# Optimization experiments

Hardware: AMD Instinct MI355X
Metric: run time of the kernel (lower is better)

The kernel has to match this reference:

```python
import jax, jax.numpy as jnp
import numpy as np

DIM = 2048
N_HEADS = 16
HEAD_DIM = DIM // N_HEADS
EPS = 1e-6


def setup_inputs() -> dict:
    key = jax.random.key(0)
    k1, k2, k3, k4, k5 = jax.random.split(key, 5)
    B, S = 2, 2048
    x = jax.random.normal(k1, (B, S, DIM), dtype=jnp.float32)
    cos = jax.random.uniform(k2, (S, HEAD_DIM), dtype=jnp.float32)
    sin = jax.random.uniform(k3, (S, HEAD_DIM), dtype=jnp.float32)
    # torch nn.Linear convention: weight [out_features, in_features], y = x @ W.T
    W_qkv = jax.random.normal(k4, (3 * DIM, DIM), dtype=jnp.float32) * 0.02
    W_proj = jax.random.normal(k5, (DIM, DIM), dtype=jnp.float32) * 0.02
    return {"x": x, "cos": cos, "sin": sin, "W_qkv": W_qkv, "W_proj": W_proj}


def _apply_rope(x, cos, sin):
    # x: [B,H,S,D], cos/sin: [S,D]; rotate interleaved even/odd pairs
    x1, x2 = x[..., ::2], x[..., 1::2]
    c = cos[:, ::2][None, None]  # [1,1,S,D/2]
    s = sin[:, ::2][None, None]
    y1 = x1 * c - x2 * s
    y2 = x1 * s + x2 * c
    return jnp.stack([y1, y2], axis=-1).reshape(x.shape)


def _rms_norm(x):
    # per-head RMS normalization over last dim, no learned scale
    return x * jax.lax.rsqrt(jnp.mean(x * x, axis=-1, keepdims=True) + EPS)


def reference(x, cos, sin, W_qkv, W_proj):
    b, s, d = x.shape
    qkv = jnp.einsum('bsd,ed->bse', x, W_qkv)  # [B,S,3*dim]
    q, k, v = jnp.split(qkv, 3, axis=-1)
    # [B,S,dim] -> [B,H,S,Dh]
    def to_heads(t):
        return t.reshape(b, s, N_HEADS, HEAD_DIM).transpose(0, 2, 1, 3)
    q, k, v = to_heads(q), to_heads(k), to_heads(v)
    q = _apply_rope(_rms_norm(q), cos, sin)
    k = _apply_rope(_rms_norm(k), cos, sin)
    scale = 1.0 / jnp.sqrt(jnp.asarray(HEAD_DIM, dtype=x.dtype))
    scores = jnp.einsum('bhqd,bhkd->bhqk', q, k) * scale  # [B,H,S,S]
    attn = jax.nn.softmax(scores, axis=-1)
    out = jnp.einsum('bhqk,bhkd->bhqd', attn, v)  # [B,H,S,Dh]
    out = out.transpose(0, 2, 1, 3).reshape(b, s, d)
    return jnp.einsum('bsd,od->bso', out, W_proj)
```

## Files before the change

kernel.cpp:

```cpp
#include <hip/hip_runtime.h>
#include <math.h>

#define BATCH 2
#define SEQ   2048
#define DIM   2048
#define NH    16
#define HD    128
#define EPS   1e-6f

typedef _Float16 f16x8 __attribute__((ext_vector_type(8)));
typedef _Float16 f16x4 __attribute__((ext_vector_type(4)));
typedef _Float16 f16x2 __attribute__((ext_vector_type(2)));
typedef float    f32x4 __attribute__((ext_vector_type(4)));

#define MFMA_F16 __builtin_amdgcn_mfma_f32_16x16x32_f16

__global__ __launch_bounds__(256) void cvt_f16(
    const float* __restrict__ in, _Float16* __restrict__ out) {
  int i = blockIdx.x * 256 + threadIdx.x;
  float4 v = ((const float4*)in)[i];
  f16x4 o;
  o[0] = (_Float16)v.x; o[1] = (_Float16)v.y;
  o[2] = (_Float16)v.z; o[3] = (_Float16)v.w;
  ((f16x4*)out)[i] = o;
}

__global__ __launch_bounds__(512, 2) void gemm_1p(
    const _Float16* __restrict__ Ag, const _Float16* __restrict__ Bg,
    float* __restrict__ C, int M, int N, int K) {
  __shared__ __align__(16) _Float16 smem[2][384][64];

  const int t = threadIdx.x;
  const int w = t >> 6, lane = t & 63;
  const int bm = blockIdx.y * 128, bn = blockIdx.x * 256;
  const int wr = (w >> 2) * 64;
  const int wc = (w & 3) * 64;
  const int quad = lane >> 4, c15 = lane & 15;

  const _Float16* baseA = Ag + (size_t)bm * K;
  const _Float16* baseB = Bg + (size_t)bn * K;

  const int lrow = lane >> 3;
  const int lswz = ((lane & 7) ^ lrow) * 8;

  const int col0 = ((0 + quad) ^ (c15 & 7)) * 8;
  const int col1 = ((4 + quad) ^ (c15 & 7)) * 8;

  f32x4 acc[4][4] = {};
  f16x8 a0[4], b0[4], a1[4], b1[4];

#define STAGE_TILE(buf, kofs)                                                  \
  {                                                                            \
    _Pragma("unroll")                                                          \
    for (int e = 0; e < 6; ++e) {                                              \
      int c = w * 6 + e;                                                       \
      int rl = c * 8 + lrow;                                                   \
      const _Float16* g = (rl < 128) ? (baseA + (size_t)rl * K)                \
                                     : (baseB + (size_t)(rl - 128) * K);       \
      __builtin_amdgcn_global_load_lds(                                        \
          (const __attribute__((address_space(1))) unsigned int*)(g + (kofs) + lswz), \
          (__attribute__((address_space(3))) unsigned int*)(&smem[buf][c * 8][0]),    \
          16, 0, 0);                                                           \
    }                                                                          \
  }

#define RD(dstA, dstB, colv, buf)                                              \
  _Pragma("unroll")                                                            \
  for (int m2 = 0; m2 < 4; ++m2)                                               \
    dstA[m2] = *(const f16x8*)(&smem[buf][wr + m2 * 16 + c15][colv]);          \
  _Pragma("unroll")                                                            \
  for (int n2 = 0; n2 < 4; ++n2)                                               \
    dstB[n2] = *(const f16x8*)(&smem[buf][128 + wc + n2 * 16 + c15][colv]);

#define MM(af, bf)                                                             \
  _Pragma("unroll")                                                            \
  for (int m2 = 0; m2 < 4; ++m2)                                               \
    _Pragma("unroll")                                                          \
    for (int n2 = 0; n2 < 4; ++n2)                                             \
      acc[m2][n2] = MFMA_F16(af[m2], bf[n2], acc[m2][n2], 0, 0, 0);

#define SB() __builtin_amdgcn_sched_barrier(0);

  STAGE_TILE(0, 0)
  asm volatile("s_waitcnt vmcnt(0)" ::: "memory");
  SB();
  __builtin_amdgcn_s_barrier();
  SB();
  STAGE_TILE(1, 64)
  RD(a0, b0, col0, 0);

  const int NT = K >> 6;
  for (int tt = 0; tt < NT; ++tt) {
    const int buf = tt & 1;
    RD(a1, b1, col1, buf);
    __builtin_amdgcn_s_setprio(1);
    MM(a0, b0);
    __builtin_amdgcn_s_setprio(0);
    asm volatile("s_waitcnt lgkmcnt(0)" ::: "memory");
    asm volatile("s_waitcnt vmcnt(0)" ::: "memory");
    SB();
    __builtin_amdgcn_s_barrier();
    SB();
    if (tt + 2 < NT) { STAGE_TILE(buf, (tt + 2) * 64) }
    if (tt + 1 < NT) { RD(a0, b0, col0, 1 - buf); }
    __builtin_amdgcn_s_setprio(1);
    MM(a1, b1);
    __builtin_amdgcn_s_setprio(0);
  }

  #pragma unroll
  for (int m2 = 0; m2 < 4; ++m2)
    #pragma unroll
    for (int n2 = 0; n2 < 4; ++n2) {
      int col = bn + wc + 16 * n2 + c15;
      #pragma unroll
      for (int r = 0; r < 4; ++r) {
        int row = bm + wr + 16 * m2 + quad * 4 + r;
        C[(size_t)row * N + col] = acc[m2][n2][r];
      }
    }
#undef STAGE_TILE
#undef RD
#undef MM
#undef SB
}

__global__ __launch_bounds__(256) void rmsrope_f16(
    const float* __restrict__ qkv, const float* __restrict__ cosb,
    const float* __restrict__ sinb, _Float16* __restrict__ Qg,
    _Float16* __restrict__ Kg) {
  const int blk = blockIdx.x;
  const int b = blk >> 11, s = blk & (SEQ - 1);
  const int wave = threadIdx.x >> 6, lane = threadIdx.x & 63;
  const float* base = qkv + (size_t)blk * (3 * DIM);
  const float c  = cosb[s * HD + 2 * lane];
  const float sn = sinb[s * HD + 2 * lane];
  #pragma unroll
  for (int h = wave; h < NH; h += 4) {
    float2 q = *(const float2*)(base + h * HD + 2 * lane);
    float2 k = *(const float2*)(base + DIM + h * HD + 2 * lane);
    float ssq = q.x * q.x + q.y * q.y;
    float ssk = k.x * k.x + k.y * k.y;
    #pragma unroll
    for (int off = 32; off >= 1; off >>= 1) {
      ssq += __shfl_xor(ssq, off, 64);
      ssk += __shfl_xor(ssk, off, 64);
    }
    float rq = rsqrtf(ssq * (1.0f / HD) + EPS);
    float rk = rsqrtf(ssk * (1.0f / HD) + EPS);
    float q1 = q.x * rq, q2 = q.y * rq;
    float k1 = k.x * rk, k2 = k.y * rk;
    float qy1 = q1 * c - q2 * sn, qy2 = q1 * sn + q2 * c;
    float ky1 = k1 * c - k2 * sn, ky2 = k1 * sn + k2 * c;
    size_t o = ((size_t)(b * NH + h) * SEQ + s) * HD + 2 * lane;
    f16x2 qo, ko;
    qo[0] = (_Float16)qy1; qo[1] = (_Float16)qy2;
    ko[0] = (_Float16)ky1; ko[1] = (_Float16)ky2;
    *(f16x2*)(Qg + o) = qo;
    *(f16x2*)(Kg + o) = ko;
  }
}

__global__ __launch_bounds__(256) void vtrans_f16(
    const float* __restrict__ qkv, _Float16* __restrict__ Vt) {
  __shared__ _Float16 L[64 * 132];
  const int t = threadIdx.x;
  const int s0 = blockIdx.x * 64, h = blockIdx.y, b = blockIdx.z;
  const float* src = qkv + ((size_t)(b * SEQ + s0)) * (3 * DIM) + 2 * DIM + h * HD;
  #pragma unroll
  for (int it = 0; it < 8; ++it) {
    int f = t + it * 256;
    int r = f >> 5, c4 = f & 31;
    float4 v = *(const float4*)(src + (size_t)r * (3 * DIM) + c4 * 4);
    f16x4 o;
    o[0] = (_Float16)v.x; o[1] = (_Float16)v.y;
    o[2] = (_Float16)v.z; o[3] = (_Float16)v.w;
    *(f16x4*)(&L[r * 132 + c4 * 4]) = o;
  }
  __syncthreads();
  const int d = t >> 1, sc = (t & 1) * 32;
  size_t dst = ((size_t)((b * NH + h) * HD + d)) * SEQ + s0 + sc;
  #pragma unroll
  for (int j = 0; j < 8; ++j) {
    f16x4 o;
    o[0] = L[(sc + 4 * j + 0) * 132 + d];
    o[1] = L[(sc + 4 * j + 1) * 132 + d];
    o[2] = L[(sc + 4 * j + 2) * 132 + d];
    o[3] = L[(sc + 4 * j + 3) * 132 + d];
    *(f16x4*)(Vt + dst + j * 4) = o;
  }
}

#define QT 128
#define KC 32

__global__ __launch_bounds__(256, 2) void flash_f16(
    const _Float16* __restrict__ Qg, const _Float16* __restrict__ Kg,
    const _Float16* __restrict__ Vtg, _Float16* __restrict__ Og) {
  __shared__ __align__(16) _Float16 sm[21504];

  const int t = threadIdx.x, w = t >> 6, lane = t & 63;
  const int quad = lane >> 4, c15 = lane & 15;
  const int bid = blockIdx.x;
  const int grp = (bid & 7) * 4 + ((bid >> 3) >> 4);
  const int qi  = (bid >> 3) & 15;
  const int bh = grp;
  const int hy = grp & (NH - 1), bz = grp >> 4;
  const int q0 = qi * QT;
  const int wr = w * 32;

  {
    const _Float16* qsrc = Qg + ((size_t)bh * SEQ + q0) * HD;
    #pragma unroll
    for (int p = 0; p < 8; ++p) {
      int ci = p * 256 + t;
      int r = ci >> 4, c8 = (ci & 15) ^ (r & 15);
      __builtin_amdgcn_global_load_lds(
          (const __attribute__((address_space(1))) unsigned int*)(qsrc + (size_t)r * HD + c8 * 8),
          (__attribute__((address_space(3))) unsigned int*)(sm + ci * 8), 16, 0, 0);
    }
  }
  __syncthreads();
  f16x8 qf[2][4];
  #pragma unroll
  for (int mf = 0; mf < 2; ++mf)
    #pragma unroll
    for (int ks = 0; ks < 4; ++ks) {
      int m = wr + mf * 16 + c15;
      int c8 = ks * 4 + quad;
      qf[mf][ks] = *(const f16x8*)(sm + (m * 16 + (c8 ^ (m & 15))) * 8);
    }
  asm volatile("s_waitcnt lgkmcnt(0)" ::: "memory");
  __builtin_amdgcn_sched_barrier(0);
  __syncthreads();

  float lrow[8];
  f32x4 oacc[2][8];
  #pragma unroll
  for (int i = 0; i < 8; ++i) lrow[i] = 0.f;
  #pragma unroll
  for (int mf = 0; mf < 2; ++mf)
    #pragma unroll
    for (int nf = 0; nf < 8; ++nf) oacc[mf][nf] = (f32x4){0.f, 0.f, 0.f, 0.f};

  const float sl = 0.12751744f;
  const float M2 = 16.322231f;
  _Float16* Pw = sm + 16384 + w * 1280;

#define STAGE_KV(buf, kk)                                                     \
  _Pragma("unroll")                                                           \
  for (int e = 0; e < 4; ++e) {                                               \
    int idx = w * 4 + e;                                                      \
    int tile = idx >> 3, p = idx & 7;                                         \
    int ci = p * 64 + lane;                                                   \
    if (tile == 0) {                                                          \
      int r = ci >> 4, c8 = (ci & 15) ^ (r & 15);                             \
      int rp = 2 * (r & 15) + (r >> 4);                                       \
      const _Float16* src = Kg +                                              \
          ((size_t)bh * SEQ + (kk) + rp) * HD + c8 * 8;                       \
      __builtin_amdgcn_global_load_lds(                                       \
          (const __attribute__((address_space(1))) unsigned int*)src,         \
          (__attribute__((address_space(3))) unsigned int*)                   \
              (sm + (buf) * 4096 + ci * 8), 16, 0, 0);                        \
    } else {                                                                  \
      int d = ci >> 2, c8 = (ci & 3) ^ (d & 3);                               \
      const _Float16* src = Vtg + (size_t)bh * HD * SEQ + (size_t)d * SEQ     \
          + (kk) + c8 * 8;                                                    \
      __builtin_amdgcn_global_load_lds(                                       \
          (const __attribute__((address_space(1))) unsigned int*)src,         \
          (__attribute__((address_space(3))) unsigned int*)                   \
              (sm + 8192 + (buf) * 4096 + ci * 8), 16, 0, 0);                 \
    }                                                                         \
  }

  STAGE_KV(0, 0)

  const int NC = SEQ / KC;
  for (int it = 0; it < NC; ++it) {
    const int cur = it & 1, cb0 = cur * 4096;
    asm volatile("s_waitcnt vmcnt(0)" ::: "memory");
    __builtin_amdgcn_sched_barrier(0);
    __builtin_amdgcn_s_barrier();
    __builtin_amdgcn_sched_barrier(0);
    if (it + 1 < NC) { STAGE_KV(1 - cur, (it + 1) * KC) }

    f32x4 accs[2][2] = {};
    #pragma unroll
    for (int nf = 0; nf < 2; ++nf) {
      f16x8 kh[4];
      #pragma unroll
      for (int ks = 0; ks < 4; ++ks) {
        int n = nf * 16 + c15;
        int c8 = ks * 4 + quad;
        kh[ks] = *(const f16x8*)(sm + cb0 + (n * 16 + (c8 ^ (n & 15))) * 8);
      }
      __builtin_amdgcn_s_setprio(1);
      #pragma unroll
      for (int ks = 0; ks < 4; ++ks) {
        accs[0][nf] = MFMA_F16(qf[0][ks], kh[ks], accs[0][nf], 0, 0, 0);
        accs[1][nf] = MFMA_F16(qf[1][ks], kh[ks], accs[1][nf], 0, 0, 0);
      }
      __builtin_amdgcn_s_setprio(0);
    }

    #pragma unroll
    for (int mf = 0; mf < 2; ++mf)
      #pragma unroll
      for (int reg = 0; reg < 4; ++reg) {
        float p0 = exp2f(fmaf(accs[mf][0][reg], sl, -M2));
        float p1 = exp2f(fmaf(accs[mf][1][reg], sl, -M2));
        lrow[mf * 4 + reg] += p0 + p1;
        int prow = mf * 16 + quad * 4 + reg;
        f16x2 pp;
        pp[0] = (_Float16)p0; pp[1] = (_Float16)p1;
        *(f16x2*)(Pw + prow * 40 + 2 * c15) = pp;
      }

    f16x8 pa0 = *(const f16x8*)(Pw + (c15) * 40 + quad * 8);
    f16x8 pa1 = *(const f16x8*)(Pw + (16 + c15) * 40 + quad * 8);
    __builtin_amdgcn_s_setprio(1);
    #pragma unroll
    for (int nf = 0; nf < 8; ++nf) {
      int dd = nf * 16 + c15;
      int slot = (dd * 4 + (quad ^ (dd & 3))) * 8;
      f16x8 vv = *(const f16x8*)(sm + 8192 + cb0 + slot);
      oacc[0][nf] = MFMA_F16(pa0, vv, oacc[0][nf], 0, 0, 0);
      oacc[1][nf] = MFMA_F16(pa1, vv, oacc[1][nf], 0, 0, 0);
    }
    __builtin_amdgcn_s_setprio(0);
  }

  #pragma unroll
  for (int i = 0; i < 8; ++i) {
    float s = lrow[i];
    #pragma unroll
    for (int off = 8; off >= 1; off >>= 1) s += __shfl_xor(s, off, 64);
    lrow[i] = s;
  }
  #pragma unroll
  for (int mf = 0; mf < 2; ++mf)
    #pragma unroll
    for (int reg = 0; reg < 4; ++reg) {
      float inv = 1.0f / lrow[mf * 4 + reg];
      int row = q0 + wr + mf * 16 + quad * 4 + reg;
      size_t ob = ((size_t)bz * SEQ + row) * DIM + hy * HD + c15;
      #pragma unroll
      for (int nf = 0; nf < 8; ++nf)
        Og[ob + nf * 16] = (_Float16)(oacc[mf][nf][reg] * inv);
    }
#undef STAGE_KV
}

extern "C" void kernel_launch(void* const* d_in, const int* in_sizes, int n_in,
                              void* d_out, int out_size, void* d_ws, size_t ws_size,
                              hipStream_t stream) {
  const float* x     = (const float*)d_in[0];
  const float* cosb  = (const float*)d_in[1];
  const float* sinb  = (const float*)d_in[2];
  const float* Wqkv  = (const float*)d_in[3];
  const float* Wproj = (const float*)d_in[4];
  float* out = (float*)d_out;

  char* ws = (char*)d_ws;
  float* qkv = (float*)ws;
  char* R = ws + 100663296;
  _Float16* x16 = (_Float16*)(R);
  _Float16* Wh  = (_Float16*)(R + 16777216);
  _Float16* Q16 = (_Float16*)(R);
  _Float16* K16 = (_Float16*)(R + 16777216);
  _Float16* Vt  = (_Float16*)(R + 50331648);
  _Float16* O16 = (_Float16*)(ws);
  _Float16* Wph = (_Float16*)(ws + 16777216);

  cvt_f16<<<8192,  256, 0, stream>>>(x, x16);
  cvt_f16<<<12288, 256, 0, stream>>>(Wqkv, Wh);
  gemm_1p<<<dim3(24, 32), 512, 0, stream>>>(x16, Wh, qkv, 4096, 6144, 2048);
  rmsrope_f16<<<4096, 256, 0, stream>>>(qkv, cosb, sinb, Q16, K16);
  vtrans_f16<<<dim3(32, NH, BATCH), 256, 0, stream>>>(qkv, Vt);
  cvt_f16<<<4096, 256, 0, stream>>>(Wproj, Wph);
  flash_f16<<<512, 256, 0, stream>>>(Q16, K16, Vt, O16);
  gemm_1p<<<dim3(8, 32), 512, 0, stream>>>(O16, Wph, out, 4096, 2048, 2048);
}
```

Baseline: 414.0 us.

## Store QKV in fp16 and merge conversion and rope/transpose launches

The QKV projection GEMM now writes its output in fp16 instead of fp32, which halves the intermediate write and the reads that follow. The three fp32-to-fp16 conversion launches become one kernel, and the RMS-norm/RoPE and V-transpose kernels become one launch that branches on block index. This cuts launch count and memory traffic, but rounds Q, K and V to fp16 before normalization, which may cost some accuracy.

```diff
diff --git a/kernel.cpp b/kernel.cpp
--- a/kernel.cpp
+++ b/kernel.cpp
@@ -15,19 +15,29 @@
 
 #define MFMA_F16 __builtin_amdgcn_mfma_f32_16x16x32_f16
 
-__global__ __launch_bounds__(256) void cvt_f16(
-    const float* __restrict__ in, _Float16* __restrict__ out) {
-  int i = blockIdx.x * 256 + threadIdx.x;
-  float4 v = ((const float4*)in)[i];
+__global__ __launch_bounds__(256) void cvt_all(
+    const float* __restrict__ x, const float* __restrict__ wqkv,
+    const float* __restrict__ wproj, _Float16* __restrict__ x16,
+    _Float16* __restrict__ wh, _Float16* __restrict__ wph) {
+  int bid = blockIdx.x;
+  const float* in;
+  _Float16* out;
+  int i;
+  if (bid < 8192)       { in = x;     out = x16; i = bid; }
+  else if (bid < 20480) { in = wqkv;  out = wh;  i = bid - 8192; }
+  else                  { in = wproj; out = wph; i = bid - 20480; }
+  int j = i * 256 + threadIdx.x;
+  float4 v = ((const float4*)in)[j];
   f16x4 o;
   o[0] = (_Float16)v.x; o[1] = (_Float16)v.y;
   o[2] = (_Float16)v.z; o[3] = (_Float16)v.w;
-  ((f16x4*)out)[i] = o;
-}
-
+  ((f16x4*)out)[j] = o;
+}
+
+template <typename OT>
 __global__ __launch_bounds__(512, 2) void gemm_1p(
     const _Float16* __restrict__ Ag, const _Float16* __restrict__ Bg,
-    float* __restrict__ C, int M, int N, int K) {
+    OT* __restrict__ C, int M, int N, int K) {
   __shared__ __align__(16) _Float16 smem[2][384][64];
 
   const int t = threadIdx.x;
@@ -116,7 +126,7 @@
       #pragma unroll
       for (int r = 0; r < 4; ++r) {
         int row = bm + wr + 16 * m2 + quad * 4 + r;
-        C[(size_t)row * N + col] = acc[m2][n2][r];
+        C[(size_t)row * N + col] = (OT)acc[m2][n2][r];
       }
     }
 #undef STAGE_TILE
@@ -125,69 +135,69 @@
 #undef SB
 }
 
-__global__ __launch_bounds__(256) void rmsrope_f16(
-    const float* __restrict__ qkv, const float* __restrict__ cosb,
+__global__ __launch_bounds__(256) void rope_vtrans(
+    const _Float16* __restrict__ qkv, const float* __restrict__ cosb,
     const float* __restrict__ sinb, _Float16* __restrict__ Qg,
-    _Float16* __restrict__ Kg) {
-  const int blk = blockIdx.x;
-  const int b = blk >> 11, s = blk & (SEQ - 1);
-  const int wave = threadIdx.x >> 6, lane = threadIdx.x & 63;
-  const float* base = qkv + (size_t)blk * (3 * DIM);
-  const float c  = cosb[s * HD + 2 * lane];
-  const float sn = sinb[s * HD + 2 * lane];
-  #pragma unroll
-  for (int h = wave; h < NH; h += 4) {
-    float2 q = *(const float2*)(base + h * HD + 2 * lane);
-    float2 k = *(const float2*)(base + DIM + h * HD + 2 * lane);
-    float ssq = q.x * q.x + q.y * q.y;
-    float ssk = k.x * k.x + k.y * k.y;
-    #pragma unroll
-    for (int off = 32; off >= 1; off >>= 1) {
-      ssq += __shfl_xor(ssq, off, 64);
-      ssk += __shfl_xor(ssk, off, 64);
-    }
-    float rq = rsqrtf(ssq * (1.0f / HD) + EPS);
-    float rk = rsqrtf(ssk * (1.0f / HD) + EPS);
-    float q1 = q.x * rq, q2 = q.y * rq;
-    float k1 = k.x * rk, k2 = k.y * rk;
-    float qy1 = q1 * c - q2 * sn, qy2 = q1 * sn + q2 * c;
-    float ky1 = k1 * c - k2 * sn, ky2 = k1 * sn + k2 * c;
-    size_t o = ((size_t)(b * NH + h) * SEQ + s) * HD + 2 * lane;
-    f16x2 qo, ko;
-    qo[0] = (_Float16)qy1; qo[1] = (_Float16)qy2;
-    ko[0] = (_Float16)ky1; ko[1] = (_Float16)ky2;
-    *(f16x2*)(Qg + o) = qo;
-    *(f16x2*)(Kg + o) = ko;
-  }
-}
-
-__global__ __launch_bounds__(256) void vtrans_f16(
-    const float* __restrict__ qkv, _Float16* __restrict__ Vt) {
+    _Float16* __restrict__ Kg, _Float16* __restrict__ Vt) {
   __shared__ _Float16 L[64 * 132];
+  const int bid = blockIdx.x;
   const int t = threadIdx.x;
-  const int s0 = blockIdx.x * 64, h = blockIdx.y, b = blockIdx.z;
-  const float* src = qkv + ((size_t)(b * SEQ + s0)) * (3 * DIM) + 2 * DIM + h * HD;
-  #pragma unroll
-  for (int it = 0; it < 8; ++it) {
-    int f = t + it * 256;
-    int r = f >> 5, c4 = f & 31;
-    float4 v = *(const float4*)(src + (size_t)r * (3 * DIM) + c4 * 4);
-    f16x4 o;
-    o[0] = (_Float16)v.x; o[1] = (_Float16)v.y;
-    o[2] = (_Float16)v.z; o[3] = (_Float16)v.w;
-    *(f16x4*)(&L[r * 132 + c4 * 4]) = o;
-  }
-  __syncthreads();
-  const int d = t >> 1, sc = (t & 1) * 32;
-  size_t dst = ((size_t)((b * NH + h) * HD + d)) * SEQ + s0 + sc;
-  #pragma unroll
-  for (int j = 0; j < 8; ++j) {
-    f16x4 o;
-    o[0] = L[(sc + 4 * j + 0) * 132 + d];
-    o[1] = L[(sc + 4 * j + 1) * 132 + d];
-    o[2] = L[(sc + 4 * j + 2) * 132 + d];
-    o[3] = L[(sc + 4 * j + 3) * 132 + d];
-    *(f16x4*)(Vt + dst + j * 4) = o;
+  if (bid < 4096) {
+    const int b = bid >> 11, s = bid & (SEQ - 1);
+    const int wave = t >> 6, lane = t & 63;
+    const _Float16* base = qkv + (size_t)bid * (3 * DIM);
+    const float c  = cosb[s * HD + 2 * lane];
+    const float sn = sinb[s * HD + 2 * lane];
+    #pragma unroll
+    for (int h = wave; h < NH; h += 4) {
+      f16x2 qv = *(const f16x2*)(base + h * HD + 2 * lane);
+      f16x2 kv = *(const f16x2*)(base + DIM + h * HD + 2 * lane);
+      float qx = (float)qv[0], qy = (float)qv[1];
+      float kx = (float)kv[0], ky = (float)kv[1];
+      float ssq = qx * qx + qy * qy;
+      float ssk = kx * kx + ky * ky;
+      #pragma unroll
+      for (int off = 32; off >= 1; off >>= 1) {
+        ssq += __shfl_xor(ssq, off, 64);
+        ssk += __shfl_xor(ssk, off, 64);
+      }
+      float rq = rsqrtf(ssq * (1.0f / HD) + EPS);
+      float rk = rsqrtf(ssk * (1.0f / HD) + EPS);
+      float q1 = qx * rq, q2 = qy * rq;
+      float k1 = kx * rk, k2 = ky * rk;
+      float qy1 = q1 * c - q2 * sn, qy2 = q1 * sn + q2 * c;
+      float ky1 = k1 * c - k2 * sn, ky2 = k1 * sn + k2 * c;
+      size_t o = ((size_t)(b * NH + h) * SEQ + s) * HD + 2 * lane;
+      f16x2 qo, ko;
+      qo[0] = (_Float16)qy1; qo[1] = (_Float16)qy2;
+      ko[0] = (_Float16)ky1; ko[1] = (_Float16)ky2;
+      *(f16x2*)(Qg + o) = qo;
+      *(f16x2*)(Kg + o) = ko;
+    }
+  } else {
+    const int vb = bid - 4096;
+    const int s0 = (vb & 31) * 64, h = (vb >> 5) & 15, b = vb >> 9;
+    const _Float16* src =
+        qkv + ((size_t)(b * SEQ + s0)) * (3 * DIM) + 2 * DIM + h * HD;
+    #pragma unroll
+    for (int it = 0; it < 4; ++it) {
+      int f = t + it * 256;
+      int r = f >> 4, c8 = f & 15;
+      f16x8 v = *(const f16x8*)(src + (size_t)r * (3 * DIM) + c8 * 8);
+      *(f16x8*)(&L[r * 132 + c8 * 8]) = v;
+    }
+    __syncthreads();
+    const int d = t >> 1, sc = (t & 1) * 32;
+    size_t dst = ((size_t)((b * NH + h) * HD + d)) * SEQ + s0 + sc;
+    #pragma unroll
+    for (int j = 0; j < 8; ++j) {
+      f16x4 o;
+      o[0] = L[(sc + 4 * j + 0) * 132 + d];
+      o[1] = L[(sc + 4 * j + 1) * 132 + d];
+      o[2] = L[(sc + 4 * j + 2) * 132 + d];
+      o[3] = L[(sc + 4 * j + 3) * 132 + d];
+      *(f16x4*)(Vt + dst + j * 4) = o;
+    }
   }
 }
 
@@ -362,22 +372,19 @@
   float* out = (float*)d_out;
 
   char* ws = (char*)d_ws;
-  float* qkv = (float*)ws;
+  _Float16* qkv16 = (_Float16*)ws;
   char* R = ws + 100663296;
   _Float16* x16 = (_Float16*)(R);
   _Float16* Wh  = (_Float16*)(R + 16777216);
+  _Float16* Wph = (_Float16*)(R + 41943040);
   _Float16* Q16 = (_Float16*)(R);
   _Float16* K16 = (_Float16*)(R + 16777216);
   _Float16* Vt  = (_Float16*)(R + 50331648);
   _Float16* O16 = (_Float16*)(ws);
-  _Float16* Wph = (_Float16*)(ws + 16777216);
-
-  cvt_f16<<<8192,  256, 0, stream>>>(x, x16);
-  cvt_f16<<<12288, 256, 0, stream>>>(Wqkv, Wh);
-  gemm_1p<<<dim3(24, 32), 512, 0, stream>>>(x16, Wh, qkv, 4096, 6144, 2048);
-  rmsrope_f16<<<4096, 256, 0, stream>>>(qkv, cosb, sinb, Q16, K16);
-  vtrans_f16<<<dim3(32, NH, BATCH), 256, 0, stream>>>(qkv, Vt);
-  cvt_f16<<<4096, 256, 0, stream>>>(Wproj, Wph);
+
+  cvt_all<<<24576, 256, 0, stream>>>(x, Wqkv, Wproj, x16, Wh, Wph);
+  gemm_1p<_Float16><<<dim3(24, 32), 512, 0, stream>>>(x16, Wh, qkv16, 4096, 6144, 2048);
+  rope_vtrans<<<5120, 256, 0, stream>>>(qkv16, cosb, sinb, Q16, K16, Vt);
   flash_f16<<<512, 256, 0, stream>>>(Q16, K16, Vt, O16);
-  gemm_1p<<<dim3(8, 32), 512, 0, stream>>>(O16, Wph, out, 4096, 2048, 2048);
-}
+  gemm_1p<float><<<dim3(8, 32), 512, 0, stream>>>(O16, Wph, out, 4096, 2048, 2048);
+}
```

Result: faster. 398.9 us (-3.7%).
